# Optimization experiments

Measured on AMD Instinct MI355X. Metric: run time of the kernel, lower is better.

The kernel has to match this reference:

```python
import jax, jax.numpy as jnp
import numpy as np

B, S, D, H, DFF = 2, 2048, 768, 12, 3072
DH = D // H
EPS = 1e-5


def _ln(x, g, b):
    m = jnp.mean(x, axis=-1, keepdims=True)
    v = jnp.mean((x - m) ** 2, axis=-1, keepdims=True)
    return (x - m) * jax.lax.rsqrt(v + EPS) * g + b


def setup_inputs() -> dict:
    key = jax.random.key(0)
    ks = jax.random.split(key, 13)
    sd = 1.0 / np.sqrt(D)
    sf = 1.0 / np.sqrt(DFF)
    return {
        "x": jax.random.normal(ks[0], (B, S, D), jnp.float32),
        "Wq": jax.random.uniform(ks[1], (D, D), jnp.float32, -sd, sd),
        "bq": jnp.zeros((D,), jnp.float32),
        "Wk": jax.random.uniform(ks[2], (D, D), jnp.float32, -sd, sd),
        "bk": jnp.zeros((D,), jnp.float32),
        "Wv": jax.random.uniform(ks[3], (D, D), jnp.float32, -sd, sd),
        "bv": jnp.zeros((D,), jnp.float32),
        "Wo": jax.random.uniform(ks[4], (D, D), jnp.float32, -sd, sd),
        "bo": jnp.zeros((D,), jnp.float32),
        "W1": jax.random.uniform(ks[5], (D, DFF), jnp.float32, -sd, sd),
        "b1": jnp.zeros((DFF,), jnp.float32),
        "W2": jax.random.uniform(ks[6], (DFF, D), jnp.float32, -sf, sf),
        "b2": jnp.zeros((D,), jnp.float32),
        "g1": jnp.ones((D,), jnp.float32),
        "be1": jnp.zeros((D,), jnp.float32),
        "g2": jnp.ones((D,), jnp.float32),
        "be2": jnp.zeros((D,), jnp.float32),
    }


def reference(x, Wq, bq, Wk, bk, Wv, bv, Wo, bo, W1, b1, W2, b2, g1, be1, g2, be2):
    # QKV projections, then split heads: [B,S,D] -> [B,H,S,DH]
    def heads(t):
        return t.reshape(B, S, H, DH).transpose(0, 2, 1, 3)
    Q = heads(x @ Wq + bq)
    K = heads(x @ Wk + bk)
    V = heads(x @ Wv + bv)
    # Per-head loop in original == batched-over-heads attention here (same math)
    scores = jnp.einsum("bhqd,bhkd->bhqk", Q, K) / np.sqrt(DH)
    attn = jax.nn.softmax(scores, axis=-1)  # [B,H,S,S] -- dominant intermediate
    ctx = jnp.einsum("bhqk,bhkd->bhqd", attn, V)
    ctx = ctx.transpose(0, 2, 1, 3).reshape(B, S, D)  # concat heads
    x = x + (ctx @ Wo + bo)
    x = _ln(x, g1, be1)
    ffn = (jax.nn.gelu(x @ W1 + b1, approximate=False)) @ W2 + b2
    x = _ln(x + ffn, g2, be2)
    return x
```

## Files before the change

kernel.cpp:

```cpp
#include <hip/hip_runtime.h>
#include <math.h>

#define BB 2
#define SS 2048
#define DD 768
#define HH 12
#define DHH 64
#define DFFN 3072
#define MTOK (BB*SS)
#define KVSPL 4

typedef __attribute__((ext_vector_type(8))) __bf16 bf16x8;
typedef __attribute__((ext_vector_type(4))) float f32x4;
typedef __attribute__((ext_vector_type(16))) float f32x16;

__device__ __forceinline__ unsigned short f2bf(float f) {
    unsigned int b = __builtin_bit_cast(unsigned int, f);
    b += 0x7FFFu + ((b >> 16) & 1u);
    return (unsigned short)(b >> 16);
}
__device__ __forceinline__ float bf2f(unsigned short u) {
    unsigned int b = ((unsigned int)u) << 16;
    return __builtin_bit_cast(float, b);
}

__device__ __forceinline__ unsigned int cvt_pk_bf16(float lo, float hi) {
    unsigned int r;
    asm("v_cvt_pk_bf16_f32 %0, %1, %2" : "=v"(r) : "v"(lo), "v"(hi));
    return r;
}

__device__ __forceinline__ void gload_lds16(const void* g, void* l) {
    __builtin_amdgcn_global_load_lds((const __attribute__((address_space(1))) unsigned int*)g,
                                     (__attribute__((address_space(3))) unsigned int*)l,
                                     16, 0, 0);
}

#if __has_builtin(__builtin_amdgcn_permlane32_swap)
__device__ __forceinline__ void pswap(unsigned int x, unsigned int y,
                                      unsigned int& r0, unsigned int& r1) {
    auto r = __builtin_amdgcn_permlane32_swap(x, y, false, false);
    r0 = r[0]; r1 = r[1];
}
#else
__device__ __forceinline__ void pswap(unsigned int x, unsigned int y,
                                      unsigned int& r0, unsigned int& r1) {
    unsigned int xs = __shfl_xor(x, 32);
    unsigned int ys = __shfl_xor(y, 32);
    bool hi = (threadIdx.x & 32) != 0;
    r0 = hi ? ys : x;
    r1 = hi ? y : xs;
}
#endif

__device__ __forceinline__ float xhalf_max(float v) {
    unsigned int u = __builtin_bit_cast(unsigned int, v);
    unsigned int a, b;
    pswap(u, u, a, b);
    return fmaxf(__builtin_bit_cast(float, a), __builtin_bit_cast(float, b));
}
__device__ __forceinline__ float xhalf_sum(float v) {
    unsigned int u = __builtin_bit_cast(unsigned int, v);
    unsigned int a, b;
    pswap(u, u, a, b);
    return __builtin_bit_cast(float, a) + __builtin_bit_cast(float, b);
}

template <int ACT, int OBF>
__global__ __launch_bounds__(256) void gemm_mfma(const unsigned short* __restrict__ A,
                                                 const unsigned short* __restrict__ Bt,
                                                 const float* __restrict__ bias,
                                                 void* __restrict__ Cout,
                                                 int M, int N, int ldA, int ldB, int Klen) {
    __shared__ unsigned short As[2 * 128 * 64];
    __shared__ unsigned short Bs[2 * 128 * 64];
    const int tid = threadIdx.x;
    const int lane = tid & 63;
    const int w = tid >> 6;
    const int l15 = lane & 15, l4 = lane >> 4;
    const int m0 = blockIdx.x * 128;
    const int n0 = blockIdx.y * 128;
    const int z = blockIdx.z;
    const int wr = (w >> 1) * 64;
    const int wc = (w & 1) * 64;

    const unsigned short* Az = A + (size_t)z * Klen;
    const unsigned short* Bz = Bt + (size_t)z * Klen;

    f32x4 acc[4][4] = {};

    int srow[4], scd[4];
#pragma unroll
    for (int i = 0; i < 4; ++i) {
        int s = w * 256 + i * 64 + lane;
        srow[i] = s >> 3;
        scd[i] = (((s & 7) ^ (srow[i] & 7))) * 8;
    }

#pragma unroll
    for (int i = 0; i < 4; ++i) {
        gload_lds16(Az + (size_t)(m0 + srow[i]) * ldA + scd[i], &As[(w * 256 + i * 64) * 8]);
        gload_lds16(Bz + (size_t)(n0 + srow[i]) * ldB + scd[i], &Bs[(w * 256 + i * 64) * 8]);
    }
    __syncthreads();

    int cb = 0;
    for (int k0 = 0; k0 < Klen; k0 += 64) {
        if (k0 + 64 < Klen) {
            const int nb = (cb ^ 1) * 128 * 64;
#pragma unroll
            for (int i = 0; i < 4; ++i) {
                gload_lds16(Az + (size_t)(m0 + srow[i]) * ldA + k0 + 64 + scd[i],
                            &As[nb + (w * 256 + i * 64) * 8]);
                gload_lds16(Bz + (size_t)(n0 + srow[i]) * ldB + k0 + 64 + scd[i],
                            &Bs[nb + (w * 256 + i * 64) * 8]);
            }
        }
        const unsigned short* Ac = &As[cb * 128 * 64];
        const unsigned short* Bc = &Bs[cb * 128 * 64];
#pragma unroll
        for (int ks = 0; ks < 2; ++ks) {
            bf16x8 af[4], bfr[4];
#pragma unroll
            for (int m = 0; m < 4; ++m) {
                int r = wr + m * 16 + l15;
                int c = (ks * 4 + l4) ^ (r & 7);
                af[m] = *(const bf16x8*)&Ac[(r * 8 + c) * 8];
            }
#pragma unroll
            for (int n = 0; n < 4; ++n) {
                int r = wc + n * 16 + l15;
                int c = (ks * 4 + l4) ^ (r & 7);
                bfr[n] = *(const bf16x8*)&Bc[(r * 8 + c) * 8];
            }
#pragma unroll
            for (int m = 0; m < 4; ++m)
#pragma unroll
                for (int n = 0; n < 4; ++n)
                    acc[m][n] = __builtin_amdgcn_mfma_f32_16x16x32_bf16(af[m], bfr[n], acc[m][n], 0, 0, 0);
        }
        __syncthreads();
        cb ^= 1;
    }

    const size_t zoff = (size_t)z * M * N;
#pragma unroll
    for (int n = 0; n < 4; ++n) {
        int col = n0 + wc + n * 16 + l15;
        float bv = bias ? bias[col] : 0.0f;
#pragma unroll
        for (int m = 0; m < 4; ++m) {
#pragma unroll
            for (int r = 0; r < 4; ++r) {
                int row = m0 + wr + m * 16 + l4 * 4 + r;
                float v = acc[m][n][r] + bv;
                if (ACT) v = 0.5f * v * (1.0f + erff(v * 0.70710678118654752f));
                if (OBF) ((unsigned short*)Cout)[(size_t)row * N + col] = f2bf(v);
                else     ((float*)Cout)[zoff + (size_t)row * N + col] = v;
            }
        }
    }
}

__global__ __launch_bounds__(256) void attn_mfma5(const unsigned short* __restrict__ QKV,
                                                  const unsigned short* __restrict__ Vt,
                                                  unsigned short* __restrict__ Opart,
                                                  float* __restrict__ ML) {
    __shared__ unsigned short Ks[2 * 64 * 64];
    __shared__ unsigned short Vs[2 * 64 * 64];
    const int tid = threadIdx.x;
    const int lane = tid & 63;
    const int w = tid >> 6;
    const int l31 = lane & 31;
    const int hi = lane >> 5;
    const int bh = blockIdx.y;
    const int b = bh / HH, h = bh % HH;
    const int z = blockIdx.z;
    const int q0 = blockIdx.x * 128 + w * 32;
    const float CLOG = 0.18033688011112042f;

    bf16x8 qf[4];
    {
        const unsigned short* qp = QKV + (size_t)(b * SS + q0 + l31) * 2304 + h * 64 + hi * 8;
        qf[0] = *(const bf16x8*)qp;
        qf[1] = *(const bf16x8*)(qp + 16);
        qf[2] = *(const bf16x8*)(qp + 32);
        qf[3] = *(const bf16x8*)(qp + 48);
    }

    f32x16 oacc[2] = {};
    float m_run = -1e30f, l_run = 0.0f;

    int arow[2], acd[2];
#pragma unroll
    for (int i = 0; i < 2; ++i) {
        int s = w * 128 + i * 64 + lane;
        arow[i] = s >> 3;
        acd[i] = ((s & 7) ^ (arow[i] & 7)) * 8;
    }

    const int kbase = z * (SS / KVSPL);
#pragma unroll
    for (int i = 0; i < 2; ++i) {
        gload_lds16(QKV + (size_t)(b * SS + kbase + arow[i]) * 2304 + DD + h * 64 + acd[i],
                    &Ks[(w * 128 + i * 64) * 8]);
        gload_lds16(Vt + (size_t)(bh * 64 + arow[i]) * SS + kbase + acd[i],
                    &Vs[(w * 128 + i * 64) * 8]);
    }
    __syncthreads();

    int cb = 0;
    const int NT = (SS / KVSPL) / 64;
    for (int it = 0; it < NT; ++it) {
        if (it + 1 < NT) {
            const int k0n = kbase + (it + 1) * 64;
            const int nb = (cb ^ 1) * 64 * 64;
#pragma unroll
            for (int i = 0; i < 2; ++i) {
                gload_lds16(QKV + (size_t)(b * SS + k0n + arow[i]) * 2304 + DD + h * 64 + acd[i],
                            &Ks[nb + (w * 128 + i * 64) * 8]);
                gload_lds16(Vt + (size_t)(bh * 64 + arow[i]) * SS + k0n + acd[i],
                            &Vs[nb + (w * 128 + i * 64) * 8]);
            }
        }
        const unsigned short* Kc = &Ks[cb * 64 * 64];
        const unsigned short* Vc = &Vs[cb * 64 * 64];

        f32x16 st[2] = {};
#pragma unroll
        for (int t = 0; t < 2; ++t) {
#pragma unroll
            for (int ks = 0; ks < 4; ++ks) {
                int row = 32 * t + l31;
                int ch = (2 * ks + hi) ^ (row & 7);
                bf16x8 kf = *(const bf16x8*)&Kc[(row * 8 + ch) * 8];
                st[t] = __builtin_amdgcn_mfma_f32_32x32x16_bf16(kf, qf[ks], st[t], 0, 0, 0);
            }
        }

        float pmax = fmaxf(st[0][0], fmaxf(st[0][1], st[0][2]));
#pragma unroll
        for (int r = 3; r < 15; r += 2) pmax = fmaxf(pmax, fmaxf(st[0][r], st[0][r + 1]));
        pmax = fmaxf(pmax, st[0][15]);
#pragma unroll
        for (int r = 0; r < 16; r += 2) pmax = fmaxf(pmax, fmaxf(st[1][r], st[1][r + 1]));
        pmax = xhalf_max(pmax) * CLOG;

        if (!__all(pmax <= m_run + 8.0f)) {
            float mn = fmaxf(m_run, pmax);
            float corr = exp2f(m_run - mn);
#pragma unroll
            for (int d = 0; d < 2; ++d)
#pragma unroll
                for (int r = 0; r < 16; ++r) oacc[d][r] *= corr;
            l_run *= corr;
            m_run = mn;
        }

        unsigned int Wn[2][4][2];
        float rs = 0.0f;
#pragma unroll
        for (int t = 0; t < 2; ++t) {
#pragma unroll
            for (int blk = 0; blk < 4; ++blk) {
                float pa = exp2f(fmaf(st[t][4 * blk + 0], CLOG, -m_run));
                float pb = exp2f(fmaf(st[t][4 * blk + 1], CLOG, -m_run));
                float pc = exp2f(fmaf(st[t][4 * blk + 2], CLOG, -m_run));
                float pd = exp2f(fmaf(st[t][4 * blk + 3], CLOG, -m_run));
                rs += (pa + pb) + (pc + pd);
                Wn[t][blk][0] = cvt_pk_bf16(pa, pb);
                Wn[t][blk][1] = cvt_pk_bf16(pc, pd);
            }
        }
        l_run += xhalf_sum(rs);

#pragma unroll
        for (int t = 0; t < 2; ++t) {
#pragma unroll
            for (int ks2 = 0; ks2 < 2; ++ks2) {
                unsigned int a0, a1, b0, b1;
                pswap(Wn[t][2 * ks2][0], Wn[t][2 * ks2 + 1][0], a0, a1);
                pswap(Wn[t][2 * ks2][1], Wn[t][2 * ks2 + 1][1], b0, b1);
                union { unsigned int u[4]; bf16x8 v; } pu;
                pu.u[0] = a0; pu.u[1] = b0;
                pu.u[2] = a1; pu.u[3] = b1;
#pragma unroll
                for (int d = 0; d < 2; ++d) {
                    int row = 32 * d + l31;
                    int ch = (4 * t + 2 * ks2 + hi) ^ (row & 7);
                    bf16x8 vf = *(const bf16x8*)&Vc[(row * 8 + ch) * 8];
                    oacc[d] = __builtin_amdgcn_mfma_f32_32x32x16_bf16(vf, pu.v, oacc[d], 0, 0, 0);
                }
            }
        }
        __syncthreads();
        cb ^= 1;
    }

    unsigned short* op = Opart + (size_t)z * MTOK * DD + (size_t)(b * SS + q0 + l31) * DD + h * 64;
#pragma unroll
    for (int d = 0; d < 2; ++d) {
#pragma unroll
        for (int blk = 0; blk < 4; ++blk) {
            unsigned int w0 = cvt_pk_bf16(oacc[d][4 * blk + 0], oacc[d][4 * blk + 1]);
            unsigned int w1 = cvt_pk_bf16(oacc[d][4 * blk + 2], oacc[d][4 * blk + 3]);
            *(unsigned long long*)(op + 32 * d + 8 * blk + 4 * hi) =
                (unsigned long long)w0 | ((unsigned long long)w1 << 32);
        }
    }
    if (hi == 0) {
        size_t mi = (((size_t)z * BB * HH + bh) * SS + (q0 + l31)) * 2;
        ML[mi] = m_run;
        ML[mi + 1] = l_run;
    }
}

__global__ __launch_bounds__(256) void attn_combine(const unsigned short* __restrict__ Opart,
                                                    const float* __restrict__ ML,
                                                    unsigned short* __restrict__ Ctx) {
    const int row = blockIdx.x;
    const int tid = threadIdx.x;
    const int b = row >> 11, s = row & 2047;
    unsigned short* co = Ctx + (size_t)row * DD;
#pragma unroll
    for (int i = 0; i < 3; ++i) {
        int c = tid + i * 256;
        int h = c >> 6;
        float m[KVSPL], l[KVSPL];
        float M = -1e30f;
#pragma unroll
        for (int zz = 0; zz < KVSPL; ++zz) {
            size_t mi = (((size_t)zz * BB * HH + b * HH + h) * SS + s) * 2;
            m[zz] = ML[mi]; l[zz] = ML[mi + 1];
            M = fmaxf(M, m[zz]);
        }
        float denom = 0.0f, num = 0.0f;
#pragma unroll
        for (int zz = 0; zz < KVSPL; ++zz) {
            float wgt = exp2f(m[zz] - M);
            denom += wgt * l[zz];
            num += wgt * bf2f(Opart[(size_t)zz * MTOK * DD + (size_t)row * DD + c]);
        }
        co[c] = f2bf(num / denom);
    }
}

__global__ __launch_bounds__(256) void v_transpose(const unsigned short* __restrict__ QKV,
                                                   unsigned short* __restrict__ Vt) {
    __shared__ unsigned short t[64][66];
    const int tid = threadIdx.x;
    const int bh = blockIdx.y, b = bh / HH, h = bh % HH;
    const int s0 = blockIdx.x * 64;
    const int c = tid & 63, r0 = tid >> 6;
#pragma unroll
    for (int i = 0; i < 16; ++i) {
        int r = i * 4 + r0;
        t[r][c] = QKV[(size_t)(b * SS + s0 + r) * 2304 + 1536 + h * 64 + c];
    }
    __syncthreads();
#pragma unroll
    for (int i = 0; i < 16; ++i) {
        int r = i * 4 + r0;
        Vt[((size_t)bh * 64 + r) * SS + s0 + c] = t[c][r];
    }
}

__device__ __forceinline__ void wtrans_body(const float* __restrict__ W,
                                            unsigned short* __restrict__ Wt,
                                            int K, int N, int rowoff,
                                            int k0, int n0, int tid,
                                            float (*t)[33]) {
    const int c = tid & 31, r0 = tid >> 5;
#pragma unroll
    for (int i = 0; i < 4; ++i) {
        int r = i * 8 + r0;
        t[r][c] = W[(size_t)(k0 + r) * N + n0 + c];
    }
    __syncthreads();
#pragma unroll
    for (int i = 0; i < 4; ++i) {
        int r = i * 8 + r0;
        Wt[(size_t)(rowoff + n0 + r) * K + k0 + c] = f2bf(t[c][r]);
    }
}

__global__ __launch_bounds__(256) void prep_all(const float* __restrict__ x,
                                                unsigned short* __restrict__ xb,
                                                const float* __restrict__ Wq,
                                                const float* __restrict__ Wk,
                                                const float* __restrict__ Wv,
                                                const float* __restrict__ Wo,
                                                const float* __restrict__ W1,
                                                const float* __restrict__ W2,
                                                unsigned short* __restrict__ Wqkvt,
                                                unsigned short* __restrict__ Wot,
                                                unsigned short* __restrict__ W1t,
                                                unsigned short* __restrict__ W2t,
                                                const float* __restrict__ bq,
                                                const float* __restrict__ bk,
                                                const float* __restrict__ bv,
                                                float* __restrict__ bqkv) {
    __shared__ float t[32][33];
    const int bid = blockIdx.x;
    const int tid = threadIdx.x;
    if (bid < 3072) {
        int i = bid * 256 + tid;
        float4 v = ((const float4*)x)[i];
        unsigned long long pk = (unsigned long long)f2bf(v.x)
                              | ((unsigned long long)f2bf(v.y) << 16)
                              | ((unsigned long long)f2bf(v.z) << 32)
                              | ((unsigned long long)f2bf(v.w) << 48);
        ((unsigned long long*)xb)[i] = pk;
    } else if (bid < 3648) {
        int lb = bid - 3072;
        wtrans_body(Wq, Wqkvt, DD, DD, 0, (lb % 24) * 32, (lb / 24) * 32, tid, t);
    } else if (bid < 4224) {
        int lb = bid - 3648;
        wtrans_body(Wk, Wqkvt, DD, DD, DD, (lb % 24) * 32, (lb / 24) * 32, tid, t);
    } else if (bid < 4800) {
        int lb = bid - 4224;
        wtrans_body(Wv, Wqkvt, DD, DD, 2 * DD, (lb % 24) * 32, (lb / 24) * 32, tid, t);
    } else if (bid < 5376) {
        int lb = bid - 4800;
        wtrans_body(Wo, Wot, DD, DD, 0, (lb % 24) * 32, (lb / 24) * 32, tid, t);
    } else if (bid < 7680) {
        int lb = bid - 5376;
        wtrans_body(W1, W1t, DD, DFFN, 0, (lb % 24) * 32, (lb / 24) * 32, tid, t);
    } else if (bid < 9984) {
        int lb = bid - 7680;
        wtrans_body(W2, W2t, DFFN, DD, 0, (lb % 96) * 32, (lb / 96) * 32, tid, t);
    } else {
        int i = (bid - 9984) * 256 + tid;
        if (i < DD) { bqkv[i] = bq[i]; bqkv[DD + i] = bk[i]; bqkv[2 * DD + i] = bv[i]; }
    }
}

template <int WB>
__global__ __launch_bounds__(256) void add_ln3(const float* __restrict__ a,
                                               const float* __restrict__ p1,
                                               const float* __restrict__ p2,
                                               const float* __restrict__ bias,
                                               const float* __restrict__ g,
                                               const float* __restrict__ be,
                                               float* __restrict__ outf,
                                               unsigned short* __restrict__ outb) {
    const int row = blockIdx.x;
    const int tid = threadIdx.x;
    float x[3];
    float s = 0.0f, s2 = 0.0f;
#pragma unroll
    for (int i = 0; i < 3; ++i) {
        int c = tid + i * 256;
        size_t idx = (size_t)row * DD + c;
        float v = a[idx] + p1[idx] + p2[idx] + bias[c];
        x[i] = v; s += v; s2 += v * v;
    }
#pragma unroll
    for (int off = 32; off; off >>= 1) {
        s += __shfl_down(s, off);
        s2 += __shfl_down(s2, off);
    }
    __shared__ float ws[8];
    const int wid = tid >> 6, lane = tid & 63;
    if (lane == 0) { ws[wid] = s; ws[4 + wid] = s2; }
    __syncthreads();
    if (tid == 0) {
        ws[0] = ws[0] + ws[1] + ws[2] + ws[3];
        ws[4] = ws[4] + ws[5] + ws[6] + ws[7];
    }
    __syncthreads();
    const float mean = ws[0] * (1.0f / DD);
    const float var = ws[4] * (1.0f / DD) - mean * mean;
    const float inv = rsqrtf(var + 1e-5f);
#pragma unroll
    for (int i = 0; i < 3; ++i) {
        int c = tid + i * 256;
        float res = (x[i] - mean) * inv * g[c] + be[c];
        outf[(size_t)row * DD + c] = res;
        if (WB) outb[(size_t)row * DD + c] = f2bf(res);
    }
}

extern "C" void kernel_launch(void* const* d_in, const int* in_sizes, int n_in,
                              void* d_out, int out_size, void* d_ws, size_t ws_size,
                              hipStream_t stream) {
    const float* x   = (const float*)d_in[0];
    const float* Wq  = (const float*)d_in[1];
    const float* bq  = (const float*)d_in[2];
    const float* Wk  = (const float*)d_in[3];
    const float* bk  = (const float*)d_in[4];
    const float* Wv  = (const float*)d_in[5];
    const float* bv  = (const float*)d_in[6];
    const float* Wo  = (const float*)d_in[7];
    const float* bo  = (const float*)d_in[8];
    const float* W1  = (const float*)d_in[9];
    const float* b1  = (const float*)d_in[10];
    const float* W2  = (const float*)d_in[11];
    const float* b2  = (const float*)d_in[12];
    const float* g1  = (const float*)d_in[13];
    const float* be1 = (const float*)d_in[14];
    const float* g2  = (const float*)d_in[15];
    const float* be2 = (const float*)d_in[16];
    float* out = (float*)d_out;

    char* w8 = (char*)d_ws;
    unsigned short* QKV = (unsigned short*)w8;
    unsigned short* Hff = (unsigned short*)w8;
    unsigned short* Vt  = (unsigned short*)(w8 + 18874368);
    unsigned short* Ctxb  = (unsigned short*)(w8 + 25165824);
    unsigned short* xb    = (unsigned short*)(w8 + 31457280);
    unsigned short* Wqkvt = (unsigned short*)(w8 + 37748736);
    unsigned short* Wot   = (unsigned short*)(w8 + 41287680);
    unsigned short* W1t   = (unsigned short*)(w8 + 42467328);
    unsigned short* W2t   = (unsigned short*)(w8 + 47185920);
    float* bqkv = (float*)(w8 + 51904512);
    unsigned short* Ob = (unsigned short*)(w8 + 51916800);
    float* Pa   = (float*)(w8 + 51916800);
    float* Pb   = (float*)(w8 + 64499712);
    float* X2   = (float*)(w8 + 77082624);
    float* ML   = (float*)(w8 + 89665536);

    dim3 blk(256);

    prep_all<<<dim3(9987), blk, 0, stream>>>(x, xb, Wq, Wk, Wv, Wo, W1, W2,
                                             Wqkvt, Wot, W1t, W2t, bq, bk, bv, bqkv);

    gemm_mfma<0, 1><<<dim3(32, 18, 1), blk, 0, stream>>>(xb, Wqkvt, bqkv, QKV,
                                                         MTOK, 3 * DD, DD, DD, DD);
    v_transpose<<<dim3(32, 24), blk, 0, stream>>>(QKV, Vt);
    attn_mfma5<<<dim3(SS / 128, BB * HH, KVSPL), blk, 0, stream>>>(QKV, Vt, Ob, ML);
    attn_combine<<<dim3(MTOK), blk, 0, stream>>>(Ob, ML, Ctxb);
    gemm_mfma<0, 0><<<dim3(32, 6, 2), blk, 0, stream>>>(Ctxb, Wot, nullptr, Pa,
                                                        MTOK, DD, DD, DD, 384);
    add_ln3<1><<<dim3(MTOK), blk, 0, stream>>>(x, Pa, Pb, bo, g1, be1, X2, xb);
    gemm_mfma<1, 1><<<dim3(32, 24, 1), blk, 0, stream>>>(xb, W1t, b1, Hff,
                                                         MTOK, DFFN, DD, DD, DD);
    gemm_mfma<0, 0><<<dim3(32, 6, 2), blk, 0, stream>>>(Hff, W2t, nullptr, Pa,
                                                        MTOK, DD, DFFN, DFFN, 1536);
    add_ln3<0><<<dim3(MTOK), blk, 0, stream>>>(X2, Pa, Pb, b2, g2, be2, out, nullptr);
}
```

Measured before the change: 333.6 us.

## Single-buffer GEMM LDS tiles and split FFN-down GEMM three ways over K

The GEMM kernel drops its double-buffered LDS prefetch in favor of a single buffer, loading each K tile between two barriers. This halves shared memory per block so more blocks can fit on a CU, but global loads no longer overlap the MFMA work. The W2 GEMM's split-K goes from 2 to 3 (K chunk 1024), and partial outputs now go to separate buffers that the LayerNorm kernel sums. The third partial reuses the Ctx region, which is dead by that point.

```diff
diff --git a/kernel.cpp b/kernel.cpp
--- a/kernel.cpp
+++ b/kernel.cpp
@@ -70,10 +70,12 @@
 __global__ __launch_bounds__(256) void gemm_mfma(const unsigned short* __restrict__ A,
                                                  const unsigned short* __restrict__ Bt,
                                                  const float* __restrict__ bias,
-                                                 void* __restrict__ Cout,
+                                                 void* __restrict__ C0,
+                                                 float* __restrict__ P1,
+                                                 float* __restrict__ P2,
                                                  int M, int N, int ldA, int ldB, int Klen) {
-    __shared__ unsigned short As[2 * 128 * 64];
-    __shared__ unsigned short Bs[2 * 128 * 64];
+    __shared__ unsigned short As[128 * 64];
+    __shared__ unsigned short Bs[128 * 64];
     const int tid = threadIdx.x;
     const int lane = tid & 63;
     const int w = tid >> 6;
@@ -86,6 +88,7 @@
 
     const unsigned short* Az = A + (size_t)z * Klen;
     const unsigned short* Bz = Bt + (size_t)z * Klen;
+    float* Pz = (z == 0) ? (float*)C0 : (z == 1 ? P1 : P2);
 
     f32x4 acc[4][4] = {};
 
@@ -97,27 +100,16 @@
         scd[i] = (((s & 7) ^ (srow[i] & 7))) * 8;
     }
 
-#pragma unroll
-    for (int i = 0; i < 4; ++i) {
-        gload_lds16(Az + (size_t)(m0 + srow[i]) * ldA + scd[i], &As[(w * 256 + i * 64) * 8]);
-        gload_lds16(Bz + (size_t)(n0 + srow[i]) * ldB + scd[i], &Bs[(w * 256 + i * 64) * 8]);
-    }
-    __syncthreads();
-
-    int cb = 0;
     for (int k0 = 0; k0 < Klen; k0 += 64) {
-        if (k0 + 64 < Klen) {
-            const int nb = (cb ^ 1) * 128 * 64;
-#pragma unroll
-            for (int i = 0; i < 4; ++i) {
-                gload_lds16(Az + (size_t)(m0 + srow[i]) * ldA + k0 + 64 + scd[i],
-                            &As[nb + (w * 256 + i * 64) * 8]);
-                gload_lds16(Bz + (size_t)(n0 + srow[i]) * ldB + k0 + 64 + scd[i],
-                            &Bs[nb + (w * 256 + i * 64) * 8]);
-            }
-        }
-        const unsigned short* Ac = &As[cb * 128 * 64];
-        const unsigned short* Bc = &Bs[cb * 128 * 64];
+        __syncthreads();
+#pragma unroll
+        for (int i = 0; i < 4; ++i) {
+            gload_lds16(Az + (size_t)(m0 + srow[i]) * ldA + k0 + scd[i],
+                        &As[(w * 256 + i * 64) * 8]);
+            gload_lds16(Bz + (size_t)(n0 + srow[i]) * ldB + k0 + scd[i],
+                        &Bs[(w * 256 + i * 64) * 8]);
+        }
+        __syncthreads();
 #pragma unroll
         for (int ks = 0; ks < 2; ++ks) {
             bf16x8 af[4], bfr[4];
@@ -125,13 +117,13 @@
             for (int m = 0; m < 4; ++m) {
                 int r = wr + m * 16 + l15;
                 int c = (ks * 4 + l4) ^ (r & 7);
-                af[m] = *(const bf16x8*)&Ac[(r * 8 + c) * 8];
+                af[m] = *(const bf16x8*)&As[(r * 8 + c) * 8];
             }
 #pragma unroll
             for (int n = 0; n < 4; ++n) {
                 int r = wc + n * 16 + l15;
                 int c = (ks * 4 + l4) ^ (r & 7);
-                bfr[n] = *(const bf16x8*)&Bc[(r * 8 + c) * 8];
+                bfr[n] = *(const bf16x8*)&Bs[(r * 8 + c) * 8];
             }
 #pragma unroll
             for (int m = 0; m < 4; ++m)
@@ -139,11 +131,8 @@
                 for (int n = 0; n < 4; ++n)
                     acc[m][n] = __builtin_amdgcn_mfma_f32_16x16x32_bf16(af[m], bfr[n], acc[m][n], 0, 0, 0);
         }
-        __syncthreads();
-        cb ^= 1;
-    }
-
-    const size_t zoff = (size_t)z * M * N;
+    }
+
 #pragma unroll
     for (int n = 0; n < 4; ++n) {
         int col = n0 + wc + n * 16 + l15;
@@ -155,8 +144,8 @@
                 int row = m0 + wr + m * 16 + l4 * 4 + r;
                 float v = acc[m][n][r] + bv;
                 if (ACT) v = 0.5f * v * (1.0f + erff(v * 0.70710678118654752f));
-                if (OBF) ((unsigned short*)Cout)[(size_t)row * N + col] = f2bf(v);
-                else     ((float*)Cout)[zoff + (size_t)row * N + col] = v;
+                if (OBF) ((unsigned short*)C0)[(size_t)row * N + col] = f2bf(v);
+                else     Pz[(size_t)row * N + col] = v;
             }
         }
     }
@@ -435,15 +424,16 @@
     }
 }
 
-template <int WB>
-__global__ __launch_bounds__(256) void add_ln3(const float* __restrict__ a,
-                                               const float* __restrict__ p1,
-                                               const float* __restrict__ p2,
-                                               const float* __restrict__ bias,
-                                               const float* __restrict__ g,
-                                               const float* __restrict__ be,
-                                               float* __restrict__ outf,
-                                               unsigned short* __restrict__ outb) {
+template <int WB, int NP>
+__global__ __launch_bounds__(256) void add_ln(const float* __restrict__ a,
+                                              const float* __restrict__ p1,
+                                              const float* __restrict__ p2,
+                                              const float* __restrict__ p3,
+                                              const float* __restrict__ bias,
+                                              const float* __restrict__ g,
+                                              const float* __restrict__ be,
+                                              float* __restrict__ outf,
+                                              unsigned short* __restrict__ outb) {
     const int row = blockIdx.x;
     const int tid = threadIdx.x;
     float x[3];
@@ -453,6 +443,7 @@
         int c = tid + i * 256;
         size_t idx = (size_t)row * DD + c;
         float v = a[idx] + p1[idx] + p2[idx] + bias[c];
+        if (NP == 3) v += p3[idx];
         x[i] = v; s += v; s2 += v * v;
     }
 #pragma unroll
@@ -509,6 +500,7 @@
     unsigned short* Vt  = (unsigned short*)(w8 + 18874368);
     unsigned short* Ctxb  = (unsigned short*)(w8 + 25165824);
     unsigned short* xb    = (unsigned short*)(w8 + 31457280);
+    float* Pc   = (float*)(w8 + 25165824);
     unsigned short* Wqkvt = (unsigned short*)(w8 + 37748736);
     unsigned short* Wot   = (unsigned short*)(w8 + 41287680);
     unsigned short* W1t   = (unsigned short*)(w8 + 42467328);
@@ -525,17 +517,17 @@
     prep_all<<<dim3(9987), blk, 0, stream>>>(x, xb, Wq, Wk, Wv, Wo, W1, W2,
                                              Wqkvt, Wot, W1t, W2t, bq, bk, bv, bqkv);
 
-    gemm_mfma<0, 1><<<dim3(32, 18, 1), blk, 0, stream>>>(xb, Wqkvt, bqkv, QKV,
+    gemm_mfma<0, 1><<<dim3(32, 18, 1), blk, 0, stream>>>(xb, Wqkvt, bqkv, QKV, nullptr, nullptr,
                                                          MTOK, 3 * DD, DD, DD, DD);
     v_transpose<<<dim3(32, 24), blk, 0, stream>>>(QKV, Vt);
     attn_mfma5<<<dim3(SS / 128, BB * HH, KVSPL), blk, 0, stream>>>(QKV, Vt, Ob, ML);
     attn_combine<<<dim3(MTOK), blk, 0, stream>>>(Ob, ML, Ctxb);
-    gemm_mfma<0, 0><<<dim3(32, 6, 2), blk, 0, stream>>>(Ctxb, Wot, nullptr, Pa,
+    gemm_mfma<0, 0><<<dim3(32, 6, 2), blk, 0, stream>>>(Ctxb, Wot, nullptr, Pa, Pb, Pb,
                                                         MTOK, DD, DD, DD, 384);
-    add_ln3<1><<<dim3(MTOK), blk, 0, stream>>>(x, Pa, Pb, bo, g1, be1, X2, xb);
-    gemm_mfma<1, 1><<<dim3(32, 24, 1), blk, 0, stream>>>(xb, W1t, b1, Hff,
+    add_ln<1, 2><<<dim3(MTOK), blk, 0, stream>>>(x, Pa, Pb, Pa, bo, g1, be1, X2, xb);
+    gemm_mfma<1, 1><<<dim3(32, 24, 1), blk, 0, stream>>>(xb, W1t, b1, Hff, nullptr, nullptr,
                                                          MTOK, DFFN, DD, DD, DD);
-    gemm_mfma<0, 0><<<dim3(32, 6, 2), blk, 0, stream>>>(Hff, W2t, nullptr, Pa,
-                                                        MTOK, DD, DFFN, DFFN, 1536);
-    add_ln3<0><<<dim3(MTOK), blk, 0, stream>>>(X2, Pa, Pb, b2, g2, be2, out, nullptr);
-}
+    gemm_mfma<0, 0><<<dim3(32, 6, 3), blk, 0, stream>>>(Hff, W2t, nullptr, Pa, Pb, Pc,
+                                                        MTOK, DD, DFFN, DFFN, 1024);
+    add_ln<0, 3><<<dim3(MTOK), blk, 0, stream>>>(X2, Pa, Pb, Pc, b2, g2, be2, out, nullptr);
+}
```

After: 310.7 us. -6.9%, faster.
